# Optimization experiments

Hardware: AMD Instinct MI355X
Metric: run time of the kernel (lower is better)

## Reference

```python
import math
import jax, jax.numpy as jnp
import numpy as np

H_DIM = 384
W_DIM = 384

# ---------- e3nn-style SO(3) generators (numpy, computed once at import) ----------

def _su2_generators(j):
    m = np.arange(-j, j)
    raising = np.diag(-np.sqrt(j * (j + 1) - m * (m + 1)), k=-1).astype(np.complex128)
    m = np.arange(-j + 1, j + 1)
    lowering = np.diag(np.sqrt(j * (j + 1) - m * (m - 1)), k=1).astype(np.complex128)
    m = np.arange(-j, j + 1)
    return np.stack([0.5 * (raising + lowering), np.diag(1j * m), -0.5j * (raising - lowering)], axis=0)

def _change_basis_real_to_complex(l):
    q = np.zeros((2 * l + 1, 2 * l + 1), dtype=np.complex128)
    for m in range(-l, 0):
        q[l + m, l + abs(m)] = 1 / 2 ** 0.5
        q[l + m, l - abs(m)] = -1j / 2 ** 0.5
    q[l, l] = 1
    for m in range(1, l + 1):
        q[l + m, l + abs(m)] = (-1) ** m / 2 ** 0.5
        q[l + m, l - abs(m)] = 1j * (-1) ** m / 2 ** 0.5
    return (-1j) ** l * q

def _so3_generators(l):
    X = _su2_generators(float(l))
    Q = _change_basis_real_to_complex(l)
    return np.real(np.conj(Q.T) @ X @ Q)  # (3, 2l+1, 2l+1) real

def _eig(X):
    # X is real skew-symmetric (normal) -> exactly diagonalizable, eigvals purely imaginary
    lam, V = np.linalg.eig(X)
    return (jnp.asarray(V.astype(np.complex64)),
            jnp.asarray(lam.astype(np.complex64)),
            jnp.asarray(np.linalg.inv(V).astype(np.complex64)))

_EIG = {}
for _l in (4, 6):
    _X = _so3_generators(_l)
    _EIG[_l] = (_eig(_X[1]), _eig(_X[0]))  # (Y-generator X[1], X-generator X[0])

TWO_PI = 2.0 * math.pi

def _expm_batch(t, eig):
    # exp(t * X) = Re(V diag(exp(t*lam)) V^-1) -- exact replacement for matrix_exp
    V, lam, Vinv = eig
    ph = jnp.exp(t.astype(jnp.complex64)[:, None] * lam)  # (B, n)
    return jnp.real(jnp.einsum('ik,bk,kj->bij', V, ph, Vinv))

def _wigner_D(l, alpha, beta, gamma):
    eigY, eigX = _EIG[l]
    a = jnp.mod(alpha, TWO_PI)
    b = jnp.mod(beta, TWO_PI)
    c = jnp.mod(gamma, TWO_PI)
    return _expm_batch(a, eigY) @ _expm_batch(b, eigX) @ _expm_batch(c, eigY)

# ---------- rotation helpers (e3nn conventions: Y-X-Y Euler angles) ----------

def _rot_y(a):
    ca, sa = jnp.cos(a), jnp.sin(a)
    o, z = jnp.ones_like(a), jnp.zeros_like(a)
    return jnp.stack([jnp.stack([ca, z, sa], -1),
                      jnp.stack([z, o, z], -1),
                      jnp.stack([-sa, z, ca], -1)], -2)

def _rot_x(a):
    ca, sa = jnp.cos(a), jnp.sin(a)
    o, z = jnp.ones_like(a), jnp.zeros_like(a)
    return jnp.stack([jnp.stack([o, z, z], -1),
                      jnp.stack([z, ca, -sa], -1),
                      jnp.stack([z, sa, ca], -1)], -2)

def _quat_to_matrix(q):
    w, x, y, z = q[..., 0], q[..., 1], q[..., 2], q[..., 3]
    return jnp.stack([
        jnp.stack([1 - 2 * (y * y + z * z), 2 * (x * y - z * w), 2 * (x * z + y * w)], -1),
        jnp.stack([2 * (x * y + z * w), 1 - 2 * (x * x + z * z), 2 * (y * z - x * w)], -1),
        jnp.stack([2 * (x * z - y * w), 2 * (y * z + x * w), 1 - 2 * (x * x + y * y)], -1)], -2)

def _matrix_to_angles(R):
    x = R[..., :, 1]  # R @ [0, 1, 0]
    xn = x / jnp.linalg.norm(x, axis=-1, keepdims=True)
    xn = jnp.clip(xn, -1.0, 1.0)
    b = jnp.arccos(xn[..., 1])
    a = jnp.arctan2(xn[..., 0], xn[..., 2])
    R2 = jnp.swapaxes(_rot_y(a) @ _rot_x(b), -1, -2) @ R
    c = jnp.arctan2(R2[..., 0, 2], R2[..., 0, 0])
    return a, b, c

# ---------- quaternion helpers ----------

def _qmul(q1, q2):
    w1, x1, y1, z1 = q1[..., 0], q1[..., 1], q1[..., 2], q1[..., 3]
    w2, x2, y2, z2 = q2[..., 0], q2[..., 1], q2[..., 2], q2[..., 3]
    return jnp.stack([w1 * w2 - x1 * x2 - y1 * y2 - z1 * z2,
                      w1 * x2 + x1 * w2 + y1 * z2 - z1 * y2,
                      w1 * y2 - x1 * z2 + y1 * w2 + z1 * x2,
                      w1 * z2 + x1 * y2 - y1 * x2 + z1 * w2], -1)

def _qconj(q):
    return q * jnp.asarray([1.0, -1.0, -1.0, -1.0], dtype=q.dtype)

def _misorientation(qc, qn, syms):
    q_rel = _qmul(qn, _qconj(qc))                                   # (H, W, 4)
    q_syms = _qmul(syms[None, None, :, :], q_rel[:, :, None, :])     # (H, W, 24, 4)
    idx = jnp.argmax(jnp.abs(q_syms[..., 0]), axis=-1)               # (H, W)
    q_rel = jnp.take_along_axis(q_syms, idx[:, :, None, None], axis=2)[:, :, 0, :]
    q_rel = jnp.where(q_rel[..., 0:1] < 0, -q_rel, q_rel)
    w = jnp.clip(q_rel[..., 0], -1.0, 1.0)
    xyz = q_rel[..., 1:]
    angle = (2.0 * jnp.arccos(w))[..., None]                          # (H, W, 1)
    s2 = jnp.clip(1.0 - w * w, 0.0, None)
    safe = s2 > 1e-12                                                 # sin_half > 1e-6
    sin_half = jnp.sqrt(jnp.where(safe, s2, 1.0))
    axis = jnp.where(safe[..., None], xyz / sin_half[..., None], 0.0)
    return angle, axis

# ---------- physics constants: 24 cubic symmetry quaternions ----------

def _cubic_symmetry_quats():
    def _mul(a, b):
        w1, x1, y1, z1 = a
        w2, x2, y2, z2 = b
        return np.array([w1 * w2 - x1 * x2 - y1 * y2 - z1 * z2,
                         w1 * x2 + x1 * w2 + y1 * z2 - z1 * y2,
                         w1 * y2 - x1 * z2 + y1 * w2 + z1 * x2,
                         w1 * z2 + x1 * y2 - y1 * x2 + z1 * w2])
    def _canon(q):
        q = q / np.linalg.norm(q)
        for v in q:
            if abs(v) > 1e-8:
                if v < 0:
                    q = -q
                break
        return tuple(np.round(q, 6)), q
    s = math.sqrt(0.5)
    group = {}
    for g in [np.array([1.0, 0.0, 0.0, 0.0]), np.array([s, s, 0.0, 0.0]), np.array([s, 0.0, 0.0, s])]:
        k, q = _canon(g)
        group[k] = q
    changed = True
    while changed:
        changed = False
        vals = list(group.values())
        for a in vals:
            for b in vals:
                k, q = _canon(_mul(a, b))
                if k not in group:
                    group[k] = q
                    changed = True
    syms = np.stack([group[k] for k in sorted(group.keys())], axis=0)
    assert syms.shape[0] == 24, syms.shape[0]
    return syms.astype(np.float32)

# ---------- forward ----------

def _forward(quats, s4, s6, fcc_syms, H, W):
    R = _quat_to_matrix(quats)
    alpha, beta, gamma = _matrix_to_angles(R)
    D4 = _wigner_D(4, alpha, beta, gamma)   # (B, 9, 9)
    D6 = _wigner_D(6, alpha, beta, gamma)   # (B, 13, 13)
    f4 = jnp.einsum('bij,j->bi', D4, s4)
    f6 = jnp.einsum('bij,j->bi', D6, s6)
    q_grid = quats.reshape(H, W, 4)
    q_right = jnp.roll(q_grid, -1, axis=1)
    q_down = jnp.roll(q_grid, -1, axis=0)
    ang_x, axis_x = _misorientation(q_grid, q_right, fcc_syms)
    ang_y, axis_y = _misorientation(q_grid, q_down, fcc_syms)
    ang_x = ang_x.at[:, -1].set(0.0)
    axis_x = axis_x.at[:, -1].set(0.0)
    ang_y = ang_y.at[-1, :].set(0.0)
    axis_y = axis_y.at[-1, :].set(0.0)
    f0 = ((ang_x + ang_y) * 0.5).reshape(-1, 1)
    f1 = ((axis_x + axis_y) * 0.5).reshape(-1, 3)
    return f0, f1, f4, f6

def setup_inputs() -> dict:
    key = jax.random.key(0)
    k1, k2, k3 = jax.random.split(key, 3)
    quats = jax.random.normal(k1, (H_DIM * W_DIM, 4), dtype=jnp.float32)
    quats = quats / jnp.linalg.norm(quats, axis=-1, keepdims=True)
    s4 = jax.random.normal(k2, (9,), dtype=jnp.float32)
    s6 = jax.random.normal(k3, (13,), dtype=jnp.float32)
    fcc_syms = jnp.asarray(_cubic_symmetry_quats())
    return {"quats": quats, "s4": s4, "s6": s6, "fcc_syms": fcc_syms, "H": H_DIM, "W": W_DIM}

def reference(quats, s4, s6, fcc_syms, H, W):
    return _forward(quats, s4, s6, fcc_syms, H, W)
```

## Files before the change

kernel.cpp:

```cpp
#include <hip/hip_runtime.h>
#include <math.h>

namespace ct {

constexpr double csqrt(double x) {
    double g = x > 1.0 ? x : 1.0;
    for (int i = 0; i < 60; ++i) g = 0.5 * (g + x / g);
    return g;
}

template <int n> struct Mat  { double a[n * n]; };
template <int n> struct CMat { double r[n * n]; double i[n * n]; };

template <int L>
constexpr CMat<2 * L + 1> makeQ() {
    constexpr int n = 2 * L + 1;
    CMat<n> Q{};
    const double s = 0.70710678118654752440;
    for (int m = 1; m <= L; ++m) {
        Q.r[(L - m) * n + (L + m)] = s;
        Q.i[(L - m) * n + (L - m)] = -s;
        const double f = (m & 1) ? -s : s;
        Q.r[(L + m) * n + (L + m)] = f;
        Q.i[(L + m) * n + (L - m)] = f;
    }
    Q.r[L * n + L] = 1.0;
    if ((L & 3) == 2)
        for (int k = 0; k < n * n; ++k) { Q.r[k] = -Q.r[k]; Q.i[k] = -Q.i[k]; }
    return Q;
}

template <int L, int G>
constexpr Mat<2 * L + 1> gen() {
    constexpr int n = 2 * L + 1;
    CMat<n> X{};
    const double j = (double)L;
    if (G == 0) {
        for (int i2 = 0; i2 < n - 1; ++i2) {
            const double m1 = -j + (double)i2;
            X.r[(i2 + 1) * n + i2] = -0.5 * csqrt(j * (j + 1.0) - m1 * (m1 + 1.0));
            const double m2 = -j + 1.0 + (double)i2;
            X.r[i2 * n + (i2 + 1)] =  0.5 * csqrt(j * (j + 1.0) - m2 * (m2 - 1.0));
        }
    } else {
        for (int i2 = 0; i2 < n; ++i2) X.i[i2 * n + i2] = -j + (double)i2;
    }
    const CMat<n> Q = makeQ<L>();
    CMat<n> M{};
    for (int r = 0; r < n; ++r)
        for (int c = 0; c < n; ++c) {
            double ar = 0.0, ai = 0.0;
            for (int k = 0; k < n; ++k) {
                ar += X.r[r*n+k]*Q.r[k*n+c] - X.i[r*n+k]*Q.i[k*n+c];
                ai += X.r[r*n+k]*Q.i[k*n+c] + X.i[r*n+k]*Q.r[k*n+c];
            }
            M.r[r*n+c] = ar; M.i[r*n+c] = ai;
        }
    Mat<n> R{};
    for (int r = 0; r < n; ++r)
        for (int c = 0; c < n; ++c) {
            double acc = 0.0;
            for (int k = 0; k < n; ++k)
                acc += Q.r[k*n+r]*M.r[k*n+c] + Q.i[k*n+r]*M.i[k*n+c];
            R.a[r*n+c] = acc;
        }
    return R;
}

template <int n>
constexpr Mat<n> mul(const Mat<n>& A, const Mat<n>& B) {
    Mat<n> C{};
    for (int r = 0; r < n; ++r)
        for (int c = 0; c < n; ++c) {
            double acc = 0.0;
            for (int k = 0; k < n; ++k) acc += A.a[r*n+k] * B.a[k*n+c];
            C.a[r*n+c] = acc;
        }
    return C;
}

template <int n>
constexpr Mat<n> ident() { Mat<n> I{}; for (int i = 0; i < n; ++i) I.a[i*n+i] = 1.0; return I; }

template <int n>
constexpr Mat<n> scaleB(const Mat<n>& X0, const Mat<n>& X1) {
    Mat<n> B{};
    const double c0 = 3.14159265358979323846 / (1.41421356237309504880 * 64.0);
    for (int k = 0; k < n * n; ++k) B.a[k] = c0 * (X0.a[k] + X1.a[k]);
    return B;
}

template <int n>
constexpr Mat<n> taylor_range(const Mat<n>& A, const Mat<n>& Pin, int khi, int klo) {
    Mat<n> P = Pin;
    for (int k = khi; k >= klo; --k) {
        Mat<n> T{};
        for (int r = 0; r < n; ++r)
            for (int c = 0; c < n; ++c) {
                double acc = 0.0;
                for (int kk = 0; kk < n; ++kk) acc += A.a[r*n+kk] * P.a[kk*n+c];
                T.a[r*n+c] = ((r == c) ? 1.0 : 0.0) + acc / (double)k;
            }
        P = T;
    }
    return P;
}

constexpr Mat<9>  X4_1g = gen<4, 1>();
constexpr Mat<13> X6_1g = gen<6, 1>();
constexpr Mat<9>  B4    = scaleB(gen<4, 0>(), X4_1g);
constexpr Mat<13> B6    = scaleB(gen<6, 0>(), X6_1g);
constexpr Mat<9>  P4t   = taylor_range(B4, ident<9>(), 12, 1);
constexpr Mat<13> P6a   = taylor_range(B6, ident<13>(), 12, 7);
constexpr Mat<13> P6t   = taylor_range(B6, P6a, 6, 1);
constexpr Mat<9>  S4a = mul(P4t, P4t);
constexpr Mat<9>  S4b = mul(S4a, S4a);
constexpr Mat<9>  S4c = mul(S4b, S4b);
constexpr Mat<9>  S4d = mul(S4c, S4c);
constexpr Mat<9>  S4e = mul(S4d, S4d);
constexpr Mat<9>  J4d = mul(S4e, S4e);
constexpr Mat<13> S6a = mul(P6t, P6t);
constexpr Mat<13> S6b = mul(S6a, S6a);
constexpr Mat<13> S6c = mul(S6b, S6b);
constexpr Mat<13> S6d = mul(S6c, S6c);
constexpr Mat<13> S6e = mul(S6d, S6d);
constexpr Mat<13> J6d = mul(S6e, S6e);

template <int L> constexpr double Jget(int r, int c) {
    if constexpr (L == 4) return J4d.a[r * 9 + c];
    else                  return J6d.a[r * 13 + c];
}
template <int L> constexpr double Sget(int m) {
    if constexpr (L == 4) return X4_1g.a[(4 - m) * 9 + (4 + m)];
    else                  return X6_1g.a[(6 - m) * 13 + (6 + m)];
}

}


template <int L, int m>
__device__ __forceinline__ void yrot_step(float* v, const float c1, const float s1,
                                          const float cm, const float sm) {
    constexpr bool pos = (ct::Sget<L>(m) > 0.0);
    const float S  = pos ? sm : -sm;
    const float vp = v[L - m], vq = v[L + m];
    v[L - m] = fmaf(cm, vp,  S * vq);
    v[L + m] = fmaf(cm, vq, -S * vp);
    if constexpr (m < L) {
        const float cn = cm * c1 - sm * s1;
        const float sn = fmaf(sm, c1, cm * s1);
        yrot_step<L, m + 1>(v, c1, s1, cn, sn);
    }
}
template <int L>
__device__ __forceinline__ void apply_yrot(float* v, const float c1, const float s1) {
    yrot_step<L, 1>(v, c1, s1, c1, s1);
}

template <int L, int r, int k>
__device__ __forceinline__ float jrow(const float* v, float acc) {
    constexpr int n = 2 * L + 1;
    if constexpr (k == n) {
        return acc;
    } else {
        constexpr double jv = ct::Jget<L>(r, k);
        if constexpr (jv > 1e-10 || jv < -1e-10)
            return jrow<L, r, k + 1>(v, fmaf((float)jv, v[k], acc));
        else
            return jrow<L, r, k + 1>(v, acc);
    }
}
template <int L, int r>
__device__ __forceinline__ void japply_rows(const float* v, float* o) {
    constexpr int n = 2 * L + 1;
    if constexpr (r < n) {
        o[r] = jrow<L, r, 0>(v, 0.0f);
        japply_rows<L, r + 1>(v, o);
    }
}
template <int L>
__device__ __forceinline__ void apply_J(float* v) {
    constexpr int n = 2 * L + 1;
    float o[n];
    japply_rows<L, 0>(v, o);
#pragma unroll
    for (int k = 0; k < n; ++k) v[k] = o[k];
}

__device__ __forceinline__ float sgnmul(float a, float b) {
    const unsigned u = (__float_as_uint(a) ^ __float_as_uint(b)) & 0x80000000u;
    return __uint_as_float(u | 0x3f800000u);
}

__device__ __forceinline__ void miso(const float4 qc, const float4 qn,
                                     float& acosw, float* ax)
{
    const float w1 = qn.x, x1 = qn.y, y1 = qn.z, z1 = qn.w;
    const float w2 = qc.x, x2 = -qc.y, y2 = -qc.z, z2 = -qc.w;
    const float rw = w1*w2 - x1*x2 - y1*y2 - z1*z2;
    const float rx = w1*x2 + x1*w2 + y1*z2 - z1*y2;
    const float ry = w1*y2 - x1*z2 + y1*w2 + z1*x2;
    const float rz = w1*z2 + x1*y2 - y1*x2 + z1*w2;

    const float aw = fabsf(rw), axv = fabsf(rx), ayv = fabsf(ry), azv = fabsf(rz);
    const bool  xgey = axv >= ayv;
    const float mxy  = xgey ? axv : ayv;
    const float nxy  = xgey ? ayv : axv;
    const float amax = fmaxf(mxy, azv);
    const float min3 = fminf(nxy, azv);
    const float sum3 = axv + ayv + azv;

    const float S2 = 0.70710678118654752440f;
    const float cA = aw;
    const float cB = amax;
    const float cC = S2 * (aw + amax);
    const float cD = S2 * (sum3 - min3);
    const float cE = 0.5f * (aw + sum3);

    float best = cA; int cls = 0;
    if (cB > best) { best = cB; cls = 1; }
    if (cC > best) { best = cC; cls = 2; }
    if (cD > best) { best = cD; cls = 3; }
    if (cE > best) { best = cE; cls = 4; }

    const bool ix = (axv == amax);
    const bool iy = !ix && (ayv == amax);
    const bool iz = !ix && !iy;
    const bool jx = (axv == min3);
    const bool jy = !jx && (ayv == min3);
    const bool jz = !jx && !jy;

    const float ri  = ix ? rx : (iy ? ry : rz);
    const float sC  = -sgnmul(rw, ri);
    const float rDi = jx ? ry : rx;
    const float rDj = (jx || jy) ? rz : ry;
    const float sD  = sgnmul(rDi, rDj);
    const float sEx = -sgnmul(rw, rx);
    const float sEy = -sgnmul(rw, ry);
    const float sEz = -sgnmul(rw, rz);

    const bool isA = (cls == 0), isB = (cls == 1), isC = (cls == 2),
               isD = (cls == 3), isE = (cls == 4);
    const float sCS = sC * S2, sDS = sD * S2;
    const float gw = isA ? 1.f : (isC ? S2 : (isE ? 0.5f : 0.f));
    const float gx = isE ? 0.5f * sEx
                   : isD ? (jx ? 0.f : S2)
                   : isC ? (ix ? sCS : 0.f)
                   : isB ? (ix ? 1.f : 0.f) : 0.f;
    const float gy = isE ? 0.5f * sEy
                   : isD ? (jz ? sDS : (jx ? S2 : 0.f))
                   : isC ? (iy ? sCS : 0.f)
                   : isB ? (iy ? 1.f : 0.f) : 0.f;
    const float gz = isE ? 0.5f * sEz
                   : isD ? (jz ? 0.f : sDS)
                   : isC ? (iz ? sCS : 0.f)
                   : isB ? (iz ? 1.f : 0.f) : 0.f;

    const float pw = gw*rw - gx*rx - gy*ry - gz*rz;
    const float px = gw*rx + gx*rw + gy*rz - gz*ry;
    const float py = gw*ry - gx*rz + gy*rw + gz*rx;
    const float pz = gw*rz + gx*ry - gy*rx + gz*rw;

    const float sgn = (pw < 0.f) ? -1.f : 1.f;
    const float w   = fminf(fabsf(pw), 1.0f);
    const float tq  = sqrtf(fmaxf(1.f - w, 0.f));
    acosw = tq * (1.5707288f + w*(-0.2121144f + w*(0.0742610f - 0.0187293f*w)));
    const float s2v = fmaxf(1.f - w * w, 0.f);
    if (s2v > 1e-12f) {
        const float inv = rsqrtf(s2v) * sgn;
        ax[0] = px * inv; ax[1] = py * inv; ax[2] = pz * inv;
    } else {
        ax[0] = 0.f; ax[1] = 0.f; ax[2] = 0.f;
    }
}

__global__ __launch_bounds__(256) void fcc_main(
    const float4* __restrict__ quats,
    const float* __restrict__ s4g, const float* __restrict__ s6g,
    float* __restrict__ out, const int N,
    const int W, const unsigned Wmagic)
{
    __shared__ float stage[25 * 256];
    const int t  = threadIdx.x;
    const int p0 = blockIdx.x * 256;
    const int i  = p0 + t;
    const bool active = i < N;

    float f0v = 0.0f;
    float f1v[3] = {0.f, 0.f, 0.f};
    float v4[9]  = {0.f};
    float v6[13] = {0.f};

    if (active) {
        const float4 q = quats[i];
        const int row = (int)(((unsigned long long)(unsigned)i * Wmagic) >> 32);
        const int col = i - row * W;

        float ac_x = 0.f, ax_x[3] = {0.f, 0.f, 0.f};
        if (col != W - 1) miso(q, quats[i + 1], ac_x, ax_x);
        float ac_y = 0.f, ax_y[3] = {0.f, 0.f, 0.f};
        if (i < N - W)    miso(q, quats[i + W], ac_y, ax_y);
        f0v    = ac_x + ac_y;
        f1v[0] = 0.5f * (ax_x[0] + ax_y[0]);
        f1v[1] = 0.5f * (ax_x[1] + ax_y[1]);
        f1v[2] = 0.5f * (ax_x[2] + ax_y[2]);

        const float qw = q.x, qx = q.y, qy = q.z, qz = q.w;
        const float R00 = 1.f - 2.f * (qy*qy + qz*qz);
        const float R01 = 2.f * (qx*qy - qz*qw);
        const float R02 = 2.f * (qx*qz + qy*qw);
        const float R11 = 1.f - 2.f * (qx*qx + qz*qz);
        const float R20 = 2.f * (qx*qz - qy*qw);
        const float R21 = 2.f * (qy*qz + qx*qw);
        const float R22 = 1.f - 2.f * (qx*qx + qy*qy);

        float c0 = R01, c1 = R11, c2 = R21;
        const float invn = rsqrtf(c0*c0 + c1*c1 + c2*c2);
        c0 *= invn; c1 *= invn; c2 *= invn;
        c1 = fminf(fmaxf(c1, -1.f), 1.f);
        const float cb = c1;
        const float sb = sqrtf(fmaxf(1.f - c1*c1, 0.f));
        const float h2 = c0*c0 + c2*c2;
        float sa, ca;
        if (h2 > 1e-30f) { const float ih = rsqrtf(h2); sa = c0*ih; ca = c2*ih; }
        else             { sa = 0.f; ca = 1.f; }
        const float gxv = ca*R00 - sa*R20;
        const float gyv = ca*R02 - sa*R22;
        const float g2 = gxv*gxv + gyv*gyv;
        float sg, cg;
        if (g2 > 1e-30f) { const float ig = rsqrtf(g2); cg = gxv*ig; sg = gyv*ig; }
        else             { cg = 1.f; sg = 0.f; }

#pragma unroll
        for (int k = 0; k < 9; ++k) v4[k] = s4g[k];
        apply_yrot<4>(v4, cg, sg);
        apply_J<4>(v4);
        apply_yrot<4>(v4, cb, sb);
        apply_J<4>(v4);
        apply_yrot<4>(v4, ca, sa);

#pragma unroll
        for (int k = 0; k < 13; ++k) v6[k] = s6g[k];
        apply_yrot<6>(v6, cg, sg);
        apply_J<6>(v6);
        apply_yrot<6>(v6, cb, sb);
        apply_J<6>(v6);
        apply_yrot<6>(v6, ca, sa);
    }

    if (active) out[i] = f0v;

    const bool fullblk = (p0 + 256 <= N);
    if (fullblk) {
        stage[3*t + 0] = f1v[0];
        stage[3*t + 1] = f1v[1];
        stage[3*t + 2] = f1v[2];
#pragma unroll
        for (int k = 0; k < 9; ++k)  stage[768  + 9*t  + k] = v4[k];
#pragma unroll
        for (int k = 0; k < 13; ++k) stage[3072 + 13*t + k] = v6[k];
        __syncthreads();
        const float4* st4 = reinterpret_cast<const float4*>(stage);
        float4* o1 = reinterpret_cast<float4*>(out + N    + 3*p0);
        float4* o4 = reinterpret_cast<float4*>(out + 4*N  + 9*p0);
        float4* o6 = reinterpret_cast<float4*>(out + 13*N + 13*p0);
        if (t < 192) o1[t] = st4[t];
#pragma unroll
        for (int r = 0; r < 2; ++r) o4[r*256 + t] = st4[192 + r*256 + t];
        if (t < 64) o4[512 + t] = st4[704 + t];
#pragma unroll
        for (int r = 0; r < 3; ++r) o6[r*256 + t] = st4[768 + r*256 + t];
        if (t < 64) o6[768 + t] = st4[1536 + t];
    } else if (active) {
        out[N + 3*i + 0] = f1v[0];
        out[N + 3*i + 1] = f1v[1];
        out[N + 3*i + 2] = f1v[2];
#pragma unroll
        for (int k = 0; k < 9; ++k)  out[4*N  + 9*i  + k] = v4[k];
#pragma unroll
        for (int k = 0; k < 13; ++k) out[13*N + 13*i + k] = v6[k];
    }
}

extern "C" void kernel_launch(void* const* d_in, const int* in_sizes, int n_in,
                              void* d_out, int out_size, void* d_ws, size_t ws_size,
                              hipStream_t stream)
{
    const float4* quats = (const float4*)d_in[0];
    const float*  s4    = (const float*)d_in[1];
    const float*  s6    = (const float*)d_in[2];
    float*        out   = (float*)d_out;

    const int N = in_sizes[0] / 4;
    int W = (int)(sqrt((double)N) + 0.5);
    if (W * W != N) W = 384;
    const unsigned Wmagic = (unsigned)(0x100000000ull / (unsigned)W + 1);

    hipLaunchKernelGGL(fcc_main, dim3((N + 255) / 256), dim3(256), 0, stream,
                       quats, s4, s6, out, N, W, Wmagic);
}
```

Before: 12.10 us.

## Split fused kernel into three role-specialized block groups per output

Replaces the single per-pixel kernel with a launch of three block groups. One group computes the misorientation features, one the l=4 Wigner rotation and one the l=6 rotation. This triples the block count, raising parallelism and occupancy, and shrinks shared memory and register pressure per block. In exchange, the quaternion loads and the Euler angle extraction are repeated in each group.

```diff
diff --git a/kernel.cpp b/kernel.cpp
--- a/kernel.cpp
+++ b/kernel.cpp
@@ -274,111 +274,134 @@
     }
 }
 
-__global__ __launch_bounds__(256) void fcc_main(
+__device__ __forceinline__ void euler_sc(const float4 q, float& ca, float& sa,
+                                         float& cb, float& sb, float& cg, float& sg)
+{
+    const float qw = q.x, qx = q.y, qy = q.z, qz = q.w;
+    const float R00 = 1.f - 2.f * (qy*qy + qz*qz);
+    const float R01 = 2.f * (qx*qy - qz*qw);
+    const float R02 = 2.f * (qx*qz + qy*qw);
+    const float R11 = 1.f - 2.f * (qx*qx + qz*qz);
+    const float R20 = 2.f * (qx*qz - qy*qw);
+    const float R21 = 2.f * (qy*qz + qx*qw);
+    const float R22 = 1.f - 2.f * (qx*qx + qy*qy);
+
+    float c0 = R01, c1 = R11, c2 = R21;
+    const float invn = rsqrtf(c0*c0 + c1*c1 + c2*c2);
+    c0 *= invn; c1 *= invn; c2 *= invn;
+    c1 = fminf(fmaxf(c1, -1.f), 1.f);
+    cb = c1;
+    sb = sqrtf(fmaxf(1.f - c1*c1, 0.f));
+    const float h2 = c0*c0 + c2*c2;
+    if (h2 > 1e-30f) { const float ih = rsqrtf(h2); sa = c0*ih; ca = c2*ih; }
+    else             { sa = 0.f; ca = 1.f; }
+    const float gxv = ca*R00 - sa*R20;
+    const float gyv = ca*R02 - sa*R22;
+    const float g2 = gxv*gxv + gyv*gyv;
+    if (g2 > 1e-30f) { const float ig = rsqrtf(g2); cg = gxv*ig; sg = gyv*ig; }
+    else             { cg = 1.f; sg = 0.f; }
+}
+
+__global__ __launch_bounds__(256) void fcc_split(
     const float4* __restrict__ quats,
     const float* __restrict__ s4g, const float* __restrict__ s6g,
-    float* __restrict__ out, const int N,
-    const int W, const unsigned Wmagic)
+    float* __restrict__ out, const int N, const int W,
+    const unsigned Wmagic, const int nblk)
 {
-    __shared__ float stage[25 * 256];
-    const int t  = threadIdx.x;
-    const int p0 = blockIdx.x * 256;
+    __shared__ float stage[13 * 256];
+    const int t = threadIdx.x;
+    int bx = blockIdx.x;
+    int role = 0;
+    if (bx >= nblk) { role = 1; bx -= nblk; }
+    if (bx >= nblk) { role = 2; bx -= nblk; }
+    const int p0 = bx * 256;
     const int i  = p0 + t;
-    const bool active = i < N;
-
-    float f0v = 0.0f;
-    float f1v[3] = {0.f, 0.f, 0.f};
-    float v4[9]  = {0.f};
-    float v6[13] = {0.f};
-
-    if (active) {
-        const float4 q = quats[i];
-        const int row = (int)(((unsigned long long)(unsigned)i * Wmagic) >> 32);
-        const int col = i - row * W;
-
-        float ac_x = 0.f, ax_x[3] = {0.f, 0.f, 0.f};
-        if (col != W - 1) miso(q, quats[i + 1], ac_x, ax_x);
-        float ac_y = 0.f, ax_y[3] = {0.f, 0.f, 0.f};
-        if (i < N - W)    miso(q, quats[i + W], ac_y, ax_y);
-        f0v    = ac_x + ac_y;
-        f1v[0] = 0.5f * (ax_x[0] + ax_y[0]);
-        f1v[1] = 0.5f * (ax_x[1] + ax_y[1]);
-        f1v[2] = 0.5f * (ax_x[2] + ax_y[2]);
-
-        const float qw = q.x, qx = q.y, qy = q.z, qz = q.w;
-        const float R00 = 1.f - 2.f * (qy*qy + qz*qz);
-        const float R01 = 2.f * (qx*qy - qz*qw);
-        const float R02 = 2.f * (qx*qz + qy*qw);
-        const float R11 = 1.f - 2.f * (qx*qx + qz*qz);
-        const float R20 = 2.f * (qx*qz - qy*qw);
-        const float R21 = 2.f * (qy*qz + qx*qw);
-        const float R22 = 1.f - 2.f * (qx*qx + qy*qy);
-
-        float c0 = R01, c1 = R11, c2 = R21;
-        const float invn = rsqrtf(c0*c0 + c1*c1 + c2*c2);
-        c0 *= invn; c1 *= invn; c2 *= invn;
-        c1 = fminf(fmaxf(c1, -1.f), 1.f);
-        const float cb = c1;
-        const float sb = sqrtf(fmaxf(1.f - c1*c1, 0.f));
-        const float h2 = c0*c0 + c2*c2;
-        float sa, ca;
-        if (h2 > 1e-30f) { const float ih = rsqrtf(h2); sa = c0*ih; ca = c2*ih; }
-        else             { sa = 0.f; ca = 1.f; }
-        const float gxv = ca*R00 - sa*R20;
-        const float gyv = ca*R02 - sa*R22;
-        const float g2 = gxv*gxv + gyv*gyv;
-        float sg, cg;
-        if (g2 > 1e-30f) { const float ig = rsqrtf(g2); cg = gxv*ig; sg = gyv*ig; }
-        else             { cg = 1.f; sg = 0.f; }
-
-#pragma unroll
-        for (int k = 0; k < 9; ++k) v4[k] = s4g[k];
-        apply_yrot<4>(v4, cg, sg);
-        apply_J<4>(v4);
-        apply_yrot<4>(v4, cb, sb);
-        apply_J<4>(v4);
-        apply_yrot<4>(v4, ca, sa);
-
-#pragma unroll
-        for (int k = 0; k < 13; ++k) v6[k] = s6g[k];
-        apply_yrot<6>(v6, cg, sg);
-        apply_J<6>(v6);
-        apply_yrot<6>(v6, cb, sb);
-        apply_J<6>(v6);
-        apply_yrot<6>(v6, ca, sa);
-    }
-
-    if (active) out[i] = f0v;
-
-    const bool fullblk = (p0 + 256 <= N);
-    if (fullblk) {
-        stage[3*t + 0] = f1v[0];
-        stage[3*t + 1] = f1v[1];
-        stage[3*t + 2] = f1v[2];
-#pragma unroll
-        for (int k = 0; k < 9; ++k)  stage[768  + 9*t  + k] = v4[k];
-#pragma unroll
-        for (int k = 0; k < 13; ++k) stage[3072 + 13*t + k] = v6[k];
-        __syncthreads();
-        const float4* st4 = reinterpret_cast<const float4*>(stage);
-        float4* o1 = reinterpret_cast<float4*>(out + N    + 3*p0);
-        float4* o4 = reinterpret_cast<float4*>(out + 4*N  + 9*p0);
-        float4* o6 = reinterpret_cast<float4*>(out + 13*N + 13*p0);
-        if (t < 192) o1[t] = st4[t];
-#pragma unroll
-        for (int r = 0; r < 2; ++r) o4[r*256 + t] = st4[192 + r*256 + t];
-        if (t < 64) o4[512 + t] = st4[704 + t];
-#pragma unroll
-        for (int r = 0; r < 3; ++r) o6[r*256 + t] = st4[768 + r*256 + t];
-        if (t < 64) o6[768 + t] = st4[1536 + t];
-    } else if (active) {
-        out[N + 3*i + 0] = f1v[0];
-        out[N + 3*i + 1] = f1v[1];
-        out[N + 3*i + 2] = f1v[2];
-#pragma unroll
-        for (int k = 0; k < 9; ++k)  out[4*N  + 9*i  + k] = v4[k];
-#pragma unroll
-        for (int k = 0; k < 13; ++k) out[13*N + 13*i + k] = v6[k];
+    const bool active  = i < N;
+    const bool fullblk = (p0 + 256 <= N) && ((N & 3) == 0);
+
+    if (role == 0) {
+        float f0v = 0.f, f1v[3] = {0.f, 0.f, 0.f};
+        if (active) {
+            const float4 q = quats[i];
+            const int row = (int)(((unsigned long long)(unsigned)i * Wmagic) >> 32);
+            const int col = i - row * W;
+            float ac_x = 0.f, ax_x[3] = {0.f, 0.f, 0.f};
+            if (col != W - 1) miso(q, quats[i + 1], ac_x, ax_x);
+            float ac_y = 0.f, ax_y[3] = {0.f, 0.f, 0.f};
+            if (i < N - W)    miso(q, quats[i + W], ac_y, ax_y);
+            f0v    = ac_x + ac_y;
+            f1v[0] = 0.5f * (ax_x[0] + ax_y[0]);
+            f1v[1] = 0.5f * (ax_x[1] + ax_y[1]);
+            f1v[2] = 0.5f * (ax_x[2] + ax_y[2]);
+            out[i] = f0v;
+        }
+        if (fullblk) {
+            stage[3*t + 0] = f1v[0];
+            stage[3*t + 1] = f1v[1];
+            stage[3*t + 2] = f1v[2];
+            __syncthreads();
+            const float4* st4 = reinterpret_cast<const float4*>(stage);
+            float4* o1 = reinterpret_cast<float4*>(out + N + 3*p0);
+            if (t < 192) o1[t] = st4[t];
+        } else if (active) {
+            out[N + 3*i + 0] = f1v[0];
+            out[N + 3*i + 1] = f1v[1];
+            out[N + 3*i + 2] = f1v[2];
+        }
+    } else if (role == 1) {
+        float v4[9] = {0.f};
+        if (active) {
+            const float4 q = quats[i];
+            float ca, sa, cb, sb, cg, sg;
+            euler_sc(q, ca, sa, cb, sb, cg, sg);
+#pragma unroll
+            for (int k = 0; k < 9; ++k) v4[k] = s4g[k];
+            apply_yrot<4>(v4, cg, sg);
+            apply_J<4>(v4);
+            apply_yrot<4>(v4, cb, sb);
+            apply_J<4>(v4);
+            apply_yrot<4>(v4, ca, sa);
+        }
+        if (fullblk) {
+#pragma unroll
+            for (int k = 0; k < 9; ++k) stage[9*t + k] = v4[k];
+            __syncthreads();
+            const float4* st4 = reinterpret_cast<const float4*>(stage);
+            float4* o4 = reinterpret_cast<float4*>(out + 4*N + 9*p0);
+#pragma unroll
+            for (int r = 0; r < 2; ++r) o4[r*256 + t] = st4[r*256 + t];
+            if (t < 64) o4[512 + t] = st4[512 + t];
+        } else if (active) {
+#pragma unroll
+            for (int k = 0; k < 9; ++k) out[4*N + 9*i + k] = v4[k];
+        }
+    } else {
+        float v6[13] = {0.f};
+        if (active) {
+            const float4 q = quats[i];
+            float ca, sa, cb, sb, cg, sg;
+            euler_sc(q, ca, sa, cb, sb, cg, sg);
+#pragma unroll
+            for (int k = 0; k < 13; ++k) v6[k] = s6g[k];
+            apply_yrot<6>(v6, cg, sg);
+            apply_J<6>(v6);
+            apply_yrot<6>(v6, cb, sb);
+            apply_J<6>(v6);
+            apply_yrot<6>(v6, ca, sa);
+        }
+        if (fullblk) {
+#pragma unroll
+            for (int k = 0; k < 13; ++k) stage[13*t + k] = v6[k];
+            __syncthreads();
+            const float4* st4 = reinterpret_cast<const float4*>(stage);
+            float4* o6 = reinterpret_cast<float4*>(out + 13*N + 13*p0);
+#pragma unroll
+            for (int r = 0; r < 3; ++r) o6[r*256 + t] = st4[r*256 + t];
+            if (t < 64) o6[768 + t] = st4[768 + t];
+        } else if (active) {
+#pragma unroll
+            for (int k = 0; k < 13; ++k) out[13*N + 13*i + k] = v6[k];
+        }
     }
 }
 
@@ -396,6 +419,7 @@
     if (W * W != N) W = 384;
     const unsigned Wmagic = (unsigned)(0x100000000ull / (unsigned)W + 1);
 
-    hipLaunchKernelGGL(fcc_main, dim3((N + 255) / 256), dim3(256), 0, stream,
-                       quats, s4, s6, out, N, W, Wmagic);
-}
+    const int nblk = (N + 255) / 256;
+    hipLaunchKernelGGL(fcc_split, dim3(3 * nblk), dim3(256), 0, stream,
+                       quats, s4, s6, out, N, W, Wmagic, nblk);
+}
```

Result: no change. 12.25 us (+1.3%).
